# Kernel optimization log

Measured on AMD Instinct MI355X. Metric: run time of the kernel, lower is better.

Reference implementation:

```python
import math
import jax, jax.numpy as jnp
import numpy as np

# ---------------- static irrep configuration ----------------
RS_IN = [(16, 0, 0), (16, 1, 0)]
RS_OUT = [(16, 0, 0), (16, 1, 0)]


def selection_rule(l_in, p_in, l_out, p_out):
    return [l for l in range(abs(l_in - l_out), l_in + l_out + 1)
            if p_out == 0 or p_in * (-1) ** l == p_out]


# ---------------- real Wigner 3j (Clebsch-Gordan) ----------------

def _su2_cg(j1, j2, j3, m1, m2, m3):
    if m1 + m2 != m3:
        return 0.0
    f = math.factorial
    pref = math.sqrt((2 * j3 + 1) * f(j3 + j1 - j2) * f(j3 - j1 + j2) * f(j1 + j2 - j3) / f(j1 + j2 + j3 + 1))
    pref *= math.sqrt(f(j3 + m3) * f(j3 - m3) * f(j1 - m1) * f(j1 + m1) * f(j2 - m2) * f(j2 + m2))
    s = 0.0
    for k in range(0, j1 + j2 - j3 + 1):
        d = [k, j1 + j2 - j3 - k, j1 - m1 - k, j2 + m2 - k, j3 - j1 - m2 + k, j3 - j2 + m1 + k]
        if any(x < 0 for x in d):
            continue
        s += (-1) ** k / np.prod([float(f(x)) for x in d])
    return pref * s


def _c2r(l):
    # real SH = A @ complex SH, rows/cols ordered m = -l..l
    A = np.zeros((2 * l + 1, 2 * l + 1), dtype=complex)
    s2 = 1.0 / math.sqrt(2)
    for m in range(-l, l + 1):
        if m < 0:
            A[l + m, l + m] = 1j * s2
            A[l + m, l - m] = -1j * (-1) ** m * s2
        elif m == 0:
            A[l, l] = 1.0
        else:
            A[l + m, l - m] = s2
            A[l + m, l + m] = (-1) ** m * s2
    return A


_W3J_CACHE = {}

def wigner_3j(l1, l2, l3):
    key = (l1, l2, l3)
    if key in _W3J_CACHE:
        return _W3J_CACHE[key]
    C = np.zeros((2 * l1 + 1, 2 * l2 + 1, 2 * l3 + 1))
    for m1 in range(-l1, l1 + 1):
        for m2 in range(-l2, l2 + 1):
            m3 = -(m1 + m2)
            if abs(m3) <= l3:
                C[l1 + m1, l2 + m2, l3 + m3] = ((-1) ** (l1 - l2 - m3) / math.sqrt(2 * l3 + 1)
                                                * _su2_cg(l1, l2, l3, m1, m2, -m3))
    T = np.einsum('ia,jb,kc,abc->ijk', _c2r(l1), _c2r(l2), _c2r(l3), C.astype(complex))
    T = T * (-1j) ** (l1 + l2 + l3)
    re, im = np.real(T), np.imag(T)
    T = re if np.abs(re).sum() >= np.abs(im).sum() else im
    n = math.sqrt(float((T ** 2).sum()))
    T = T / n if n > 1e-12 else T
    _W3J_CACHE[key] = T
    return T


# ---------------- real spherical harmonics (l = 0,1,2) ----------------

def real_sh(ls, xyz):
    r = jnp.linalg.norm(xyz, axis=-1)
    n = xyz / jnp.where(r > 0, r, 1.0)[..., None]
    x, y, z = n[..., 0], n[..., 1], n[..., 2]
    out = []
    for l in ls:
        if l == 0:
            out.append(jnp.full(x.shape, 0.28209479177387814, x.dtype)[None])
        elif l == 1:
            c = 0.4886025119029199
            out.append(jnp.stack([c * y, c * z, c * x]))
        elif l == 2:
            c1 = 1.0925484305920792
            c2 = 0.31539156525252005
            c3 = 0.5462742152960396
            out.append(jnp.stack([c1 * x * y, c1 * y * z, c2 * (3 * z * z - 1), c1 * x * z, c3 * (x * x - y * y)]))
        else:
            raise NotImplementedError
    return jnp.concatenate(out, axis=0)  # [sum(2l+1), batch, a, b]


def _norm_coef_table():
    nc = np.zeros((len(RS_OUT), len(RS_IN), 2))
    for i, (mul_out, l_out, p_out) in enumerate(RS_OUT):
        num = sum(mul_in * len(selection_rule(l_in, p_in, l_out, p_out))
                  for (mul_in, l_in, p_in) in RS_IN)
        for j, (mul_in, l_in, p_in) in enumerate(RS_IN):
            lm = math.sqrt(2 * l_in + 1) * math.sqrt(4 * math.pi)
            nc[i, j, 0] = lm / math.sqrt(num)
            nc[i, j, 1] = lm / math.sqrt(mul_in)
    return nc


def kernel_conv(features, geometry, mask, W1, b1, W2, b2):
    batch, a, b, _ = geometry.shape
    set_of_l_filters = sorted({l for (_, li, pi) in RS_IN for (_, lo, po) in RS_OUT
                               for l in selection_rule(li, pi, lo, po)})
    Y = real_sh(set_of_l_filters, geometry)             # [9, z, a, b]
    radii = jnp.linalg.norm(geometry, axis=-1)          # [z, a, b]
    # radial MLP: 1 -> H -> n_path
    h = jax.nn.relu(radii[..., None] * W1[0] + b1)
    R = h @ W2 + b2                                     # [z, a, b, n_path]
    nc = _norm_coef_table()
    is_zero = radii == 0

    out_blocks = []
    begin_R = 0
    for i, (mul_out, l_out, p_out) in enumerate(RS_OUT):
        block = jnp.zeros((batch, a, mul_out, 2 * l_out + 1), features.dtype)
        begin_in = 0
        for j, (mul_in, l_in, p_in) in enumerate(RS_IN):
            s_in = slice(begin_in, begin_in + mul_in * (2 * l_in + 1))
            begin_in += mul_in * (2 * l_in + 1)
            l_filters = selection_rule(l_in, p_in, l_out, p_out)
            if not l_filters:
                continue
            n = mul_out * mul_in * len(l_filters)
            sub_R = R[..., begin_R:begin_R + n].reshape(batch, a, b, mul_out, mul_in, len(l_filters))
            begin_R += n
            sub_nc = jnp.where(is_zero, nc[i, j, 1], nc[i, j, 0]).astype(features.dtype)
            f_in = features[..., s_in].reshape(batch, b, mul_in, 2 * l_in + 1)
            for k, l_f in enumerate(l_filters):
                offset = sum(2 * l + 1 for l in set_of_l_filters if l < l_f)
                sub_Y = Y[offset:offset + 2 * l_f + 1]
                C = jnp.asarray(wigner_3j(l_out, l_in, l_f), features.dtype)
                block = block + jnp.einsum('ijk,kzab,zabuv,zab,zbvj->zaui',
                                           C, sub_Y, sub_R[..., k], sub_nc, f_in)
        out_blocks.append(block.reshape(batch, a, -1))
    out = jnp.concatenate(out_blocks, axis=-1)          # [z, a, n_out]
    return out * mask[..., None]


def setup_inputs() -> dict:
    key = jax.random.key(0)
    ks = jax.random.split(key, 6)
    batch, a, b = 2, 160, 160
    dim_in, n_path, H = 64, 1536, 64
    return {
        'features': jax.random.normal(ks[0], (batch, b, dim_in), jnp.float32),
        'geometry': jax.random.normal(ks[1], (batch, a, b, 3), jnp.float32),
        'mask': jnp.ones((batch, b), jnp.float32),
        'W1': jax.random.normal(ks[2], (1, H), jnp.float32) * 0.5,
        'b1': jax.random.normal(ks[3], (H,), jnp.float32) * 0.1,
        'W2': jax.random.normal(ks[4], (H, n_path), jnp.float32) / np.sqrt(H),
        'b2': jnp.zeros((n_path,), jnp.float32),
    }


def reference(features, geometry, mask, W1, b1, W2, b2):
    return kernel_conv(features, geometry, mask, W1, b1, W2, b2)
```

## Files before the change

kernel.cpp:

```cpp
#include <hip/hip_runtime.h>
#include <hip/hip_fp16.h>
#include <math.h>

#define NPATH 1536
#define NSEG  65
#define NB    160
#define NA    160
#define CW    32
#define PPW   5

__device__ float  dg_thr[64];
__device__ float4 dg_tbl4[NSEG * 512];

static __device__ __forceinline__ __half2 bc_h2(float x) {
    union { float f; __half2 h; } u; u.f = x; return u.h;
}
static __device__ __forceinline__ unsigned short h_us(__half h) {
    union { __half h; unsigned short s; } u; u.h = h; return u.s;
}

__global__ __launch_bounds__(256) void k_prep(const float* __restrict__ W1,
                                              const float* __restrict__ b1,
                                              const float* __restrict__ W2,
                                              const float* __restrict__ b2,
                                              float* __restrict__ out) {
    int bid = blockIdx.x, tid = threadIdx.x;
    if (bid >= 390) {
        out[(bid - 390) * 256 + tid] = 0.0f;
        return;
    }
    int tseg = bid / 6, tcol = bid % 6;
    __shared__ float tv[64], mw[64], mb[64];
    if (tid < 64) {
        float w = W1[tid], b = b1[tid];
        tv[tid] = (w != 0.0f) ? (-b / w) : __builtin_inff();
    }
    __syncthreads();
    if (tid < 64) {
        float mine = tv[tid];
        int rank = 0;
        for (int j = 0; j < 64; ++j) {
            float o = tv[j];
            rank += (o < mine || (o == mine && j < tid)) ? 1 : 0;
        }
        float w = W1[tid], b = b1[tid];
        bool act = (w > 0.0f) ? (rank < tseg)
                 : (w < 0.0f) ? (rank >= tseg)
                              : (b > 0.0f);
        mw[tid] = act ? w : 0.0f;
        mb[tid] = act ? b : 0.0f;
        if (bid == 0) dg_thr[tid] = mine;
    }
    __syncthreads();

    int p = tcol * 256 + tid;
    int e, k; float scl;
    if (p < 768) {
        int u = (p >> 4) & 15, v = p & 15, vu = v * 16 + u;
        if (p < 256)      { e = vu;       k = 0; scl = 0.17677669529663687f; }
        else if (p < 512) { e = vu;       k = 1; scl = 0.6266570686577502f;  }
        else              { e = 256 + vu; k = 0; scl = 0.2558286876965162f;  }
    } else {
        int m = (p - 768) / 3, kk = (p - 768) % 3;
        int u = m >> 4, v = m & 15, vu = v * 16 + u;
        e = 256 + vu;
        if (kk == 0)      { k = 1; scl = 0.125f;              }
        else if (kk == 1) { k = 2; scl = 0.3133285343288751f; }
        else              { k = 3; scl = 0.7674950309598664f; }
    }

    float A = 0.0f, B = 0.0f;
    #pragma unroll 8
    for (int c = 0; c < 64; ++c) {
        float w2 = W2[c * NPATH + p];
        A = fmaf(mw[c], w2, A);
        B = fmaf(mb[c], w2, B);
    }
    float sv = scl * A;
    float iv = scl * (B + b2[p]);

    unsigned short* ub = (unsigned short*)dg_tbl4 + ((size_t)tseg * 512 + e) * 8;
    ub[k]     = h_us(__float2half(sv));
    ub[4 + k] = h_us(__float2half(iv));
    if (p < 256) {
        ((unsigned int*)ub)[1] = 0u;
        ((unsigned int*)ub)[3] = 0u;
    }
}

__global__ __launch_bounds__(256, 4) void k_main(const float* __restrict__ feat,
                                                 const float* __restrict__ geom,
                                                 const float* __restrict__ mask,
                                                 float* __restrict__ out) {
    int wv   = threadIdx.x >> 6;
    int lane = threadIdx.x & 63;
    int gw   = blockIdx.x * 4 + wv;
    int chunk = gw & (CW - 1);
    int za    = gw >> 5;
    int z     = za / NA;

    __shared__ __align__(16) float sFeat[4][PPW][64];
    __shared__ float sAcc[4][64];

    int h    = lane >> 5;
    int l32  = lane & 31;
    bool tl0 = l32 < 16;
    int  tu  = l32 & 15;
    int  e_base = (tl0 ? 0 : 256) + h * 16 + tu;
    float zft = tl0 ? 1.4142135623730951f : 2.0f;

    int waddr = (lane < 16) ? (lane * 4 + 3)
                            : (((lane - 16) / 3) * 4 + ((lane - 16) % 3));

    float thrv = dg_thr[lane];

    const float is30 = 0.18257418583505536f;
    const float is10 = 0.31622776601683794f;
    const float c1sh = 0.4886025119029199f;
    const float c21 = 1.0925484305920792f, c22 = 0.31539156525252005f, c23 = 0.5462742152960396f;

    int b0 = chunk * PPW;
    #pragma unroll
    for (int it = 0; it < PPW; ++it) {
        float fv = feat[((size_t)(z * NB + b0 + it)) * 64 + lane];
        sFeat[wv][it][waddr] = fv;
    }

    float rr[PPW], nxa[PPW], nya[PPW], nza[PPW], zfa[PPW];
    int rowo[PPW];
    #pragma unroll
    for (int it = 0; it < PPW; ++it) {
        const float* g = geom + ((size_t)za * NB + b0 + it) * 3;
        float gx = g[0], gy = g[1], gz = g[2];
        float r = sqrtf(gx * gx + gy * gy + gz * gz);
        bool zr = (r == 0.0f);
        float inv = zr ? 1.0f : (1.0f / r);
        nxa[it] = gx * inv; nya[it] = gy * inv; nza[it] = gz * inv;
        rr[it] = r;
        zfa[it] = zr ? zft : 1.0f;
        unsigned long long bm = __ballot(thrv < r);
        rowo[it] = __popcll(bm) * 512;
    }

    float acc0 = 0.0f, acc1 = 0.0f, acc2 = 0.0f;

    float4 tb[2][8];
    {
        const float4* __restrict__ rp0 = dg_tbl4 + rowo[0] + e_base;
        #pragma unroll
        for (int s = 0; s < 8; ++s) tb[0][s] = rp0[s * 32];
    }

    #pragma unroll
    for (int it = 0; it < PPW; ++it) {
        if (it + 1 < PPW) {
            const float4* __restrict__ rpn = dg_tbl4 + rowo[it + 1] + e_base;
            #pragma unroll
            for (int s = 0; s < 8; ++s) tb[(it + 1) & 1][s] = rpn[s * 32];
        }

        float r = rr[it];
        const float* spL = &sFeat[wv][it][0] + h * 4;
        float T0 = 0.0f;
        float T1x = 0.0f, T1y = 0.0f, T1z = 0.0f;
        float T2x = 0.0f, T2y = 0.0f, T2z = 0.0f;
        float T3x = 0.0f, T3y = 0.0f, T3z = 0.0f;
        #pragma unroll
        for (int s = 0; s < 8; ++s) {
            float4 t = tb[it & 1][s];
            __half2 hs01 = bc_h2(t.x), hs23 = bc_h2(t.y);
            __half2 hi01 = bc_h2(t.z), hi23 = bc_h2(t.w);
            float R0 = fmaf(r, __low2float(hs01),  __low2float(hi01));
            float R1 = fmaf(r, __high2float(hs01), __high2float(hi01));
            float R2 = fmaf(r, __low2float(hs23),  __low2float(hi23));
            float R3 = fmaf(r, __high2float(hs23), __high2float(hi23));
            float4 fq = *(const float4*)&spL[s * 8];
            T0  = fmaf(R0, fq.w, T0);
            T1x = fmaf(R1, fq.x, T1x);
            T1y = fmaf(R1, fq.y, T1y);
            T1z = fmaf(R1, fq.z, T1z);
            T2x = fmaf(R2, fq.x, T2x);
            T2y = fmaf(R2, fq.y, T2y);
            T2z = fmaf(R2, fq.z, T2z);
            T3x = fmaf(R3, fq.x, T3x);
            T3y = fmaf(R3, fq.y, T3y);
            T3z = fmaf(R3, fq.z, T3z);
        }

        float nx = nxa[it], ny = nya[it], nz = nza[it];
        float Y1_0 = c1sh * ny, Y1_1 = c1sh * nz, Y1_2 = c1sh * nx;
        float Y2_0 = c21 * nx * ny;
        float Y2_1 = c21 * ny * nz;
        float Y2_2 = c22 * fmaf(3.0f, nz * nz, -1.0f);
        float Y2_3 = c21 * nx * nz;
        float Y2_4 = c23 * (nx * nx - ny * ny);
        float za_ = is10 * Y2_0, zb_ = is10 * Y2_1, zc_ = is10 * Y2_3;
        float zd_ = is30 * Y2_2, ze_ = is10 * Y2_4;

        float sl0 = T0;
        sl0 = fmaf(Y1_0, T1x, sl0);
        sl0 = fmaf(Y1_1, T1y, sl0);
        sl0 = fmaf(Y1_2, T1z, sl0);

        float sx = fmaf(Y1_0, T0, T1x);
        sx = fmaf(Y1_2, T2y, sx); sx = fmaf(-Y1_1, T2z, sx);
        sx = fmaf(-(zd_ + ze_), T3x, sx); sx = fmaf(zb_, T3y, sx); sx = fmaf(za_, T3z, sx);

        float sy = fmaf(Y1_1, T0, T1y);
        sy = fmaf(-Y1_2, T2x, sy); sy = fmaf(Y1_0, T2z, sy);
        sy = fmaf(zb_, T3x, sy); sy = fmaf(2.0f * zd_, T3y, sy); sy = fmaf(zc_, T3z, sy);

        float sz = fmaf(Y1_2, T0, T1z);
        sz = fmaf(Y1_1, T2x, sz); sz = fmaf(-Y1_0, T2y, sz);
        sz = fmaf(za_, T3x, sz); sz = fmaf(zc_, T3y, sz); sz = fmaf(ze_ - zd_, T3z, sz);

        float s0 = tl0 ? sl0 : sx;
        float zf = zfa[it];
        acc0 = fmaf(s0, zf, acc0);
        acc1 = fmaf(sy, zf, acc1);
        acc2 = fmaf(sz, zf, acc2);
    }

    acc0 += __shfl_xor(acc0, 32);
    acc1 += __shfl_xor(acc1, 32);
    acc2 += __shfl_xor(acc2, 32);

    if (lane < 32) {
        if (tl0) {
            sAcc[wv][tu] = acc0;
        } else {
            int ob = 16 + tu * 3;
            sAcc[wv][ob]     = acc0;
            sAcc[wv][ob + 1] = acc1;
            sAcc[wv][ob + 2] = acc2;
        }
    }
    __syncthreads();
    if (threadIdx.x < 64) {
        float sum = sAcc[0][threadIdx.x] + sAcc[1][threadIdx.x]
                  + sAcc[2][threadIdx.x] + sAcc[3][threadIdx.x];
        sum *= mask[za];
        atomicAdd(&out[(size_t)za * 64 + threadIdx.x], sum);
    }
}

extern "C" void kernel_launch(void* const* d_in, const int* in_sizes, int n_in,
                              void* d_out, int out_size, void* d_ws, size_t ws_size,
                              hipStream_t stream) {
    (void)in_sizes; (void)n_in; (void)d_ws; (void)ws_size; (void)out_size;
    const float* feat = (const float*)d_in[0];
    const float* geom = (const float*)d_in[1];
    const float* mask = (const float*)d_in[2];
    const float* W1   = (const float*)d_in[3];
    const float* b1   = (const float*)d_in[4];
    const float* W2   = (const float*)d_in[5];
    const float* b2   = (const float*)d_in[6];
    float* out = (float*)d_out;

    k_prep<<<470, 256, 0, stream>>>(W1, b1, W2, b2, out);
    k_main<<<2 * NA * CW / 4, 256, 0, stream>>>(feat, geom, mask, out);
}
```

Measured before the change: 92.12 us.

## Precontract features into per-source piecewise-linear tables, shrinking main kernel inner loop

The prep kernel now folds the input features into the radial MLP weights for every source atom, building a per-(batch, source) table of slope and intercept for each of 65 ReLU segments. The segment tables are built incrementally by adding one hidden unit at a time in threshold order. The main kernel then loads one uint4 per lane per neighbour instead of eight float4 table rows plus shared-memory features, and does only a small spherical-harmonic combine. The cost is a larger prep step with a 320x65x256 workspace table, and fp16 storage of the contracted values, which may change numerical error.

```diff
diff --git a/kernel.cpp b/kernel.cpp
--- a/kernel.cpp
+++ b/kernel.cpp
@@ -3,94 +3,136 @@
 #include <math.h>
 
 #define NPATH 1536
-#define NSEG  65
+#define SEGS  65
 #define NB    160
 #define NA    160
 #define CW    32
 #define PPW   5
 
-__device__ float  dg_thr[64];
-__device__ float4 dg_tbl4[NSEG * 512];
-
-static __device__ __forceinline__ __half2 bc_h2(float x) {
-    union { float f; __half2 h; } u; u.f = x; return u.h;
-}
-static __device__ __forceinline__ unsigned short h_us(__half h) {
-    union { __half h; unsigned short s; } u; u.h = h; return u.s;
-}
-
-__global__ __launch_bounds__(256) void k_prep(const float* __restrict__ W1,
-                                              const float* __restrict__ b1,
-                                              const float* __restrict__ W2,
-                                              const float* __restrict__ b2,
-                                              float* __restrict__ out) {
+__device__ float dg_thr[64];
+
+#define SCL_A 0.17677669529663687f
+#define SCL_B 0.6266570686577502f
+#define SCL_C 0.2558286876965162f
+#define SCL_D 0.125f
+#define SCL_E 0.3133285343288751f
+#define SCL_F 0.7674950309598664f
+
+__global__ __launch_bounds__(128) void k_pc(const float* __restrict__ feat,
+                                            const float* __restrict__ W1,
+                                            const float* __restrict__ b1,
+                                            const float* __restrict__ W2,
+                                            const float* __restrict__ b2,
+                                            unsigned int* __restrict__ PC,
+                                            float* __restrict__ out) {
     int bid = blockIdx.x, tid = threadIdx.x;
-    if (bid >= 390) {
-        out[(bid - 390) * 256 + tid] = 0.0f;
+    if (bid >= 640) {
+        out[(bid - 640) * 128 + tid] = 0.0f;
         return;
     }
-    int tseg = bid / 6, tcol = bid % 6;
-    __shared__ float tv[64], mw[64], mb[64];
+    int zb = bid >> 1, half = bid & 1;
+    int t  = half * 128 + tid;
+
+    __shared__ float fL[64], tvL[64], iwL[64], ibL[64], dwL[64], dbL[64];
+    __shared__ int   ordL[64];
+    __shared__ float hL[64][128];
+
     if (tid < 64) {
-        float w = W1[tid], b = b1[tid];
-        tv[tid] = (w != 0.0f) ? (-b / w) : __builtin_inff();
+        fL[tid] = feat[(size_t)zb * 64 + tid];
+        float w = W1[tid], bb = b1[tid];
+        tvL[tid] = (w != 0.0f) ? (-bb / w) : __builtin_inff();
     }
     __syncthreads();
     if (tid < 64) {
-        float mine = tv[tid];
+        float mine = tvL[tid];
         int rank = 0;
-        for (int j = 0; j < 64; ++j) {
-            float o = tv[j];
-            rank += (o < mine || (o == mine && j < tid)) ? 1 : 0;
-        }
-        float w = W1[tid], b = b1[tid];
-        bool act = (w > 0.0f) ? (rank < tseg)
-                 : (w < 0.0f) ? (rank >= tseg)
-                              : (b > 0.0f);
-        mw[tid] = act ? w : 0.0f;
-        mb[tid] = act ? b : 0.0f;
+        for (int j2 = 0; j2 < 64; ++j2) {
+            float o = tvL[j2];
+            rank += (o < mine || (o == mine && j2 < tid)) ? 1 : 0;
+        }
+        float w = W1[tid], bb = b1[tid];
+        iwL[tid] = (w < 0.0f) ? w : 0.0f;
+        ibL[tid] = (w < 0.0f) ? bb : ((w == 0.0f && bb > 0.0f) ? bb : 0.0f);
+        ordL[rank] = tid;
+        dwL[rank]  = fabsf(w);
+        dbL[rank]  = (w > 0.0f) ? bb : ((w < 0.0f) ? -bb : 0.0f);
         if (bid == 0) dg_thr[tid] = mine;
     }
     __syncthreads();
 
-    int p = tcol * 256 + tid;
-    int e, k; float scl;
-    if (p < 768) {
-        int u = (p >> 4) & 15, v = p & 15, vu = v * 16 + u;
-        if (p < 256)      { e = vu;       k = 0; scl = 0.17677669529663687f; }
-        else if (p < 512) { e = vu;       k = 1; scl = 0.6266570686577502f;  }
-        else              { e = 256 + vu; k = 0; scl = 0.2558286876965162f;  }
+    int lane4 = t >> 2, j = t & 3;
+    int pbase = 0, pstr = 1, comp = -1;
+    float scl = 0.0f;
+    if (lane4 < 16) {
+        if (j == 0) { pbase = lane4 * 16;        scl = SCL_A; }
+        else        { pbase = 256 + lane4 * 16;  comp = j - 1; scl = SCL_B; }
     } else {
-        int m = (p - 768) / 3, kk = (p - 768) % 3;
-        int u = m >> 4, v = m & 15, vu = v * 16 + u;
-        e = 256 + vu;
-        if (kk == 0)      { k = 1; scl = 0.125f;              }
-        else if (kk == 1) { k = 2; scl = 0.3133285343288751f; }
-        else              { k = 3; scl = 0.7674950309598664f; }
-    }
-
-    float A = 0.0f, B = 0.0f;
-    #pragma unroll 8
+        int lu = lane4 - 16, u = lu / 3, part = lu - u * 3;
+        if (part == 0) {
+            if (j == 0) { pbase = 512 + u * 16;             scl = SCL_C; }
+            else        { pbase = 768 + u * 48; pstr = 3; comp = j - 1; scl = SCL_D; }
+        } else if (part == 1) {
+            if (j < 3)  { pbase = 768 + u * 48 + 1; pstr = 3; comp = j; scl = SCL_E; }
+        } else {
+            if (j < 3)  { pbase = 768 + u * 48 + 2; pstr = 3; comp = j; scl = SCL_F; }
+        }
+    }
+
+    float fv[16];
+    #pragma unroll
+    for (int v = 0; v < 16; ++v)
+        fv[v] = scl * ((comp < 0) ? fL[v] : fL[16 + v * 3 + comp]);
+
+    float ib2 = 0.0f;
+    #pragma unroll
+    for (int v = 0; v < 16; ++v) ib2 = fmaf(b2[pbase + v * pstr], fv[v], ib2);
+
+    float slope = 0.0f, icpt = ib2;
+    #pragma unroll 2
     for (int c = 0; c < 64; ++c) {
-        float w2 = W2[c * NPATH + p];
-        A = fmaf(mw[c], w2, A);
-        B = fmaf(mb[c], w2, B);
-    }
-    float sv = scl * A;
-    float iv = scl * (B + b2[p]);
-
-    unsigned short* ub = (unsigned short*)dg_tbl4 + ((size_t)tseg * 512 + e) * 8;
-    ub[k]     = h_us(__float2half(sv));
-    ub[4 + k] = h_us(__float2half(iv));
-    if (p < 256) {
-        ((unsigned int*)ub)[1] = 0u;
-        ((unsigned int*)ub)[3] = 0u;
-    }
-}
-
-__global__ __launch_bounds__(256, 4) void k_main(const float* __restrict__ feat,
-                                                 const float* __restrict__ geom,
+        const float* w2r = W2 + c * NPATH + pbase;
+        float h = 0.0f;
+        if (pstr == 1) {
+            const float4* q = (const float4*)w2r;
+            #pragma unroll
+            for (int v4 = 0; v4 < 4; ++v4) {
+                float4 w4 = q[v4];
+                h = fmaf(w4.x, fv[v4 * 4 + 0], h);
+                h = fmaf(w4.y, fv[v4 * 4 + 1], h);
+                h = fmaf(w4.z, fv[v4 * 4 + 2], h);
+                h = fmaf(w4.w, fv[v4 * 4 + 3], h);
+            }
+        } else {
+            #pragma unroll
+            for (int v = 0; v < 16; ++v) h = fmaf(w2r[v * 3], fv[v], h);
+        }
+        hL[c][tid] = h;
+        slope = fmaf(iwL[c], h, slope);
+        icpt  = fmaf(ibL[c], h, icpt);
+    }
+
+    unsigned int* rowp = PC + (size_t)zb * (SEGS * 256) + t;
+    union { __half2 h; unsigned int u; } pk;
+    pk.h = __halves2half2(__float2half(slope), __float2half(icpt));
+    rowp[0] = pk.u;
+    for (int s = 1; s < SEGS; ++s) {
+        int c = ordL[s - 1];
+        float h = hL[c][tid];
+        slope = fmaf(dwL[s - 1], h, slope);
+        icpt  = fmaf(dbL[s - 1], h, icpt);
+        pk.h = __halves2half2(__float2half(slope), __float2half(icpt));
+        rowp[(size_t)s * 256] = pk.u;
+    }
+}
+
+static __device__ __forceinline__ float rcomb(unsigned int v, float r) {
+    union { unsigned int u; __half2 h; } cv; cv.u = v;
+    return fmaf(r, __low2float(cv.h), __high2float(cv.h));
+}
+
+__global__ __launch_bounds__(256, 4) void k_main(const float* __restrict__ geom,
                                                  const float* __restrict__ mask,
+                                                 const unsigned int* __restrict__ PC,
                                                  float* __restrict__ out) {
     int wv   = threadIdx.x >> 6;
     int lane = threadIdx.x & 63;
@@ -99,19 +141,12 @@
     int za    = gw >> 5;
     int z     = za / NA;
 
-    __shared__ __align__(16) float sFeat[4][PPW][64];
     __shared__ float sAcc[4][64];
 
-    int h    = lane >> 5;
-    int l32  = lane & 31;
-    bool tl0 = l32 < 16;
-    int  tu  = l32 & 15;
-    int  e_base = (tl0 ? 0 : 256) + h * 16 + tu;
-    float zft = tl0 ? 1.4142135623730951f : 2.0f;
-
-    int waddr = (lane < 16) ? (lane * 4 + 3)
-                            : (((lane - 16) / 3) * 4 + ((lane - 16) % 3));
-
+    bool l0 = lane < 16;
+    int  u = 0, part = 0;
+    if (!l0) { int lu = lane - 16; u = lu / 3; part = lu - u * 3; }
+    float zft = l0 ? 1.4142135623730951f : 2.0f;
     float thrv = dg_thr[lane];
 
     const float is30 = 0.18257418583505536f;
@@ -120,14 +155,8 @@
     const float c21 = 1.0925484305920792f, c22 = 0.31539156525252005f, c23 = 0.5462742152960396f;
 
     int b0 = chunk * PPW;
-    #pragma unroll
-    for (int it = 0; it < PPW; ++it) {
-        float fv = feat[((size_t)(z * NB + b0 + it)) * 64 + lane];
-        sFeat[wv][it][waddr] = fv;
-    }
-
     float rr[PPW], nxa[PPW], nya[PPW], nza[PPW], zfa[PPW];
-    int rowo[PPW];
+    unsigned int rowo[PPW];
     #pragma unroll
     for (int it = 0; it < PPW; ++it) {
         const float* g = geom + ((size_t)za * NB + b0 + it) * 3;
@@ -139,101 +168,77 @@
         rr[it] = r;
         zfa[it] = zr ? zft : 1.0f;
         unsigned long long bm = __ballot(thrv < r);
-        rowo[it] = __popcll(bm) * 512;
+        int s = __popcll(bm);
+        rowo[it] = ((unsigned)(z * NB + b0 + it) * SEGS + (unsigned)s) * 256u
+                 + (unsigned)(lane * 4);
     }
 
     float acc0 = 0.0f, acc1 = 0.0f, acc2 = 0.0f;
 
-    float4 tb[2][8];
-    {
-        const float4* __restrict__ rp0 = dg_tbl4 + rowo[0] + e_base;
-        #pragma unroll
-        for (int s = 0; s < 8; ++s) tb[0][s] = rp0[s * 32];
-    }
+    uint4 tb[2];
+    tb[0] = *(const uint4*)(PC + rowo[0]);
 
     #pragma unroll
     for (int it = 0; it < PPW; ++it) {
-        if (it + 1 < PPW) {
-            const float4* __restrict__ rpn = dg_tbl4 + rowo[it + 1] + e_base;
-            #pragma unroll
-            for (int s = 0; s < 8; ++s) tb[(it + 1) & 1][s] = rpn[s * 32];
-        }
-
+        if (it + 1 < PPW) tb[(it + 1) & 1] = *(const uint4*)(PC + rowo[it + 1]);
+        uint4 tt = tb[it & 1];
         float r = rr[it];
-        const float* spL = &sFeat[wv][it][0] + h * 4;
-        float T0 = 0.0f;
-        float T1x = 0.0f, T1y = 0.0f, T1z = 0.0f;
-        float T2x = 0.0f, T2y = 0.0f, T2z = 0.0f;
-        float T3x = 0.0f, T3y = 0.0f, T3z = 0.0f;
-        #pragma unroll
-        for (int s = 0; s < 8; ++s) {
-            float4 t = tb[it & 1][s];
-            __half2 hs01 = bc_h2(t.x), hs23 = bc_h2(t.y);
-            __half2 hi01 = bc_h2(t.z), hi23 = bc_h2(t.w);
-            float R0 = fmaf(r, __low2float(hs01),  __low2float(hi01));
-            float R1 = fmaf(r, __high2float(hs01), __high2float(hi01));
-            float R2 = fmaf(r, __low2float(hs23),  __low2float(hi23));
-            float R3 = fmaf(r, __high2float(hs23), __high2float(hi23));
-            float4 fq = *(const float4*)&spL[s * 8];
-            T0  = fmaf(R0, fq.w, T0);
-            T1x = fmaf(R1, fq.x, T1x);
-            T1y = fmaf(R1, fq.y, T1y);
-            T1z = fmaf(R1, fq.z, T1z);
-            T2x = fmaf(R2, fq.x, T2x);
-            T2y = fmaf(R2, fq.y, T2y);
-            T2z = fmaf(R2, fq.z, T2z);
-            T3x = fmaf(R3, fq.x, T3x);
-            T3y = fmaf(R3, fq.y, T3y);
-            T3z = fmaf(R3, fq.z, T3z);
-        }
+        float T0 = rcomb(tt.x, r);
+        float T1 = rcomb(tt.y, r);
+        float T2 = rcomb(tt.z, r);
+        float T3 = rcomb(tt.w, r);
 
         float nx = nxa[it], ny = nya[it], nz = nza[it];
         float Y1_0 = c1sh * ny, Y1_1 = c1sh * nz, Y1_2 = c1sh * nx;
-        float Y2_0 = c21 * nx * ny;
-        float Y2_1 = c21 * ny * nz;
-        float Y2_2 = c22 * fmaf(3.0f, nz * nz, -1.0f);
-        float Y2_3 = c21 * nx * nz;
-        float Y2_4 = c23 * (nx * nx - ny * ny);
-        float za_ = is10 * Y2_0, zb_ = is10 * Y2_1, zc_ = is10 * Y2_3;
-        float zd_ = is30 * Y2_2, ze_ = is10 * Y2_4;
-
-        float sl0 = T0;
-        sl0 = fmaf(Y1_0, T1x, sl0);
-        sl0 = fmaf(Y1_1, T1y, sl0);
-        sl0 = fmaf(Y1_2, T1z, sl0);
-
-        float sx = fmaf(Y1_0, T0, T1x);
-        sx = fmaf(Y1_2, T2y, sx); sx = fmaf(-Y1_1, T2z, sx);
-        sx = fmaf(-(zd_ + ze_), T3x, sx); sx = fmaf(zb_, T3y, sx); sx = fmaf(za_, T3z, sx);
-
-        float sy = fmaf(Y1_1, T0, T1y);
-        sy = fmaf(-Y1_2, T2x, sy); sy = fmaf(Y1_0, T2z, sy);
-        sy = fmaf(zb_, T3x, sy); sy = fmaf(2.0f * zd_, T3y, sy); sy = fmaf(zc_, T3z, sy);
-
-        float sz = fmaf(Y1_2, T0, T1z);
-        sz = fmaf(Y1_1, T2x, sz); sz = fmaf(-Y1_0, T2y, sz);
-        sz = fmaf(za_, T3x, sz); sz = fmaf(zc_, T3y, sz); sz = fmaf(ze_ - zd_, T3z, sz);
-
-        float s0 = tl0 ? sl0 : sx;
         float zf = zfa[it];
-        acc0 = fmaf(s0, zf, acc0);
-        acc1 = fmaf(sy, zf, acc1);
-        acc2 = fmaf(sz, zf, acc2);
-    }
-
-    acc0 += __shfl_xor(acc0, 32);
-    acc1 += __shfl_xor(acc1, 32);
-    acc2 += __shfl_xor(acc2, 32);
-
-    if (lane < 32) {
-        if (tl0) {
-            sAcc[wv][tu] = acc0;
+
+        if (l0) {
+            float sl0 = T0;
+            sl0 = fmaf(Y1_0, T1, sl0);
+            sl0 = fmaf(Y1_1, T2, sl0);
+            sl0 = fmaf(Y1_2, T3, sl0);
+            acc0 = fmaf(sl0, zf, acc0);
+        } else if (part == 0) {
+            float px = fmaf(Y1_0, T0, T1);
+            float py = fmaf(Y1_1, T0, T2);
+            float pz = fmaf(Y1_2, T0, T3);
+            acc0 = fmaf(px, zf, acc0);
+            acc1 = fmaf(py, zf, acc1);
+            acc2 = fmaf(pz, zf, acc2);
+        } else if (part == 1) {
+            float px = fmaf(Y1_2, T1, -Y1_1 * T2);
+            float py = fmaf(Y1_0, T2, -Y1_2 * T0);
+            float pz = fmaf(Y1_1, T0, -Y1_0 * T1);
+            acc0 = fmaf(px, zf, acc0);
+            acc1 = fmaf(py, zf, acc1);
+            acc2 = fmaf(pz, zf, acc2);
         } else {
-            int ob = 16 + tu * 3;
-            sAcc[wv][ob]     = acc0;
-            sAcc[wv][ob + 1] = acc1;
-            sAcc[wv][ob + 2] = acc2;
-        }
+            float Y2_0 = c21 * nx * ny;
+            float Y2_1 = c21 * ny * nz;
+            float Y2_2 = c22 * fmaf(3.0f, nz * nz, -1.0f);
+            float Y2_3 = c21 * nx * nz;
+            float Y2_4 = c23 * (nx * nx - ny * ny);
+            float za_ = is10 * Y2_0, zb_ = is10 * Y2_1, zc_ = is10 * Y2_3;
+            float zd_ = is30 * Y2_2, ze_ = is10 * Y2_4;
+            float px = fmaf(-(zd_ + ze_), T0, fmaf(zb_, T1, za_ * T2));
+            float py = fmaf(zb_, T0, fmaf(2.0f * zd_, T1, zc_ * T2));
+            float pz = fmaf(za_, T0, fmaf(zc_, T1, (ze_ - zd_) * T2));
+            acc0 = fmaf(px, zf, acc0);
+            acc1 = fmaf(py, zf, acc1);
+            acc2 = fmaf(pz, zf, acc2);
+        }
+    }
+
+    float ax = acc0 + __shfl_down(acc0, 1) + __shfl_down(acc0, 2);
+    float ay = acc1 + __shfl_down(acc1, 1) + __shfl_down(acc1, 2);
+    float az = acc2 + __shfl_down(acc2, 1) + __shfl_down(acc2, 2);
+    if (l0) {
+        sAcc[wv][lane] = acc0;
+    } else if (part == 0) {
+        int ob = 16 + u * 3;
+        sAcc[wv][ob]     = ax;
+        sAcc[wv][ob + 1] = ay;
+        sAcc[wv][ob + 2] = az;
     }
     __syncthreads();
     if (threadIdx.x < 64) {
@@ -247,7 +252,7 @@
 extern "C" void kernel_launch(void* const* d_in, const int* in_sizes, int n_in,
                               void* d_out, int out_size, void* d_ws, size_t ws_size,
                               hipStream_t stream) {
-    (void)in_sizes; (void)n_in; (void)d_ws; (void)ws_size; (void)out_size;
+    (void)in_sizes; (void)n_in; (void)ws_size; (void)out_size;
     const float* feat = (const float*)d_in[0];
     const float* geom = (const float*)d_in[1];
     const float* mask = (const float*)d_in[2];
@@ -256,7 +261,8 @@
     const float* W2   = (const float*)d_in[5];
     const float* b2   = (const float*)d_in[6];
     float* out = (float*)d_out;
-
-    k_prep<<<470, 256, 0, stream>>>(W1, b1, W2, b2, out);
-    k_main<<<2 * NA * CW / 4, 256, 0, stream>>>(feat, geom, mask, out);
-}
+    unsigned int* PC = (unsigned int*)d_ws;
+
+    k_pc<<<800, 128, 0, stream>>>(feat, W1, b1, W2, b2, PC, out);
+    k_main<<<2 * NA * CW / 4, 256, 0, stream>>>(geom, mask, PC, out);
+}
```

Result: slower. 130.0 us (+41.1%).
